# Kernel tuning notes

Hardware: AMD Instinct MI355X
Metric: run time of the kernel (lower is better)

The kernel has to match this reference:

```python
import jax, jax.numpy as jnp
import numpy as np

B, S = 256, 1024
Q_IN, K_IN, V_DIM = 256, 256, 256
KEY_DIM, N_HEADS = 64, 8


def setup_inputs() -> dict:
    key = jax.random.key(0)
    ks = jax.random.split(key, 7)
    queries = jax.random.normal(ks[0], (B, Q_IN), dtype=jnp.float32)
    keys = jax.random.normal(ks[1], (B, S, K_IN), dtype=jnp.float32)
    values = jax.random.normal(ks[2], (B, S, V_DIM), dtype=jnp.float32)
    # per-head Linear params (torch Linear: y = x @ W.T + b), stacked over heads
    sq = 1.0 / np.sqrt(Q_IN)
    sk = 1.0 / np.sqrt(K_IN)
    Wq = jax.random.uniform(ks[3], (N_HEADS, KEY_DIM, Q_IN), minval=-sq, maxval=sq, dtype=jnp.float32)
    bq = jax.random.uniform(ks[4], (N_HEADS, KEY_DIM), minval=-sq, maxval=sq, dtype=jnp.float32)
    Wk = jax.random.uniform(ks[5], (N_HEADS, KEY_DIM, K_IN), minval=-sk, maxval=sk, dtype=jnp.float32)
    bk = jax.random.uniform(ks[6], (N_HEADS, KEY_DIM), minval=-sk, maxval=sk, dtype=jnp.float32)
    return {"queries": queries, "keys": keys, "values": values,
            "Wq": Wq, "bq": bq, "Wk": Wk, "bk": bk}


def reference(queries, keys, values, Wq, bq, Wk, bk):
    # q: (B, H, D)  -- single query per batch element, per head
    q = jnp.einsum('bi,hdi->bhd', queries, Wq) + bq[None, :, :]
    # k: (B, H, S, D)
    k = jnp.einsum('bsi,hdi->bhsd', keys, Wk) + bk[None, :, None, :]
    scale = 1.0 / jnp.sqrt(jnp.float32(KEY_DIM))
    # scores: (B, H, S)
    scores = jnp.einsum('bhd,bhsd->bhs', q, k) * scale
    attn = jax.nn.softmax(scores, axis=-1)
    # out: (B, H, V); original returns (B, H, 1, V) after unsqueeze+cat
    out = jnp.einsum('bhs,bsv->bhv', attn, values)
    return out[:, :, None, :]
```

## Files before the change

### kernel.cpp

```cpp
#include <hip/hip_runtime.h>

#define NHEADS 8
#define DHEAD 64
#define CIN 256
#define SLEN 1024
#define VDIM 256
#define PT_STRIDE 1048

typedef __attribute__((ext_vector_type(8))) short bf16x8;
typedef __attribute__((ext_vector_type(4))) float f32x4;

__device__ __forceinline__ unsigned short f2bf(float x) {
    unsigned int u = __builtin_bit_cast(unsigned int, x);
    u += 0x7fffu + ((u >> 16) & 1u);
    return (unsigned short)(u >> 16);
}

extern "C" __global__ void __launch_bounds__(1024)
attn_fused_kernel(const float* __restrict__ queries,
                  const float* __restrict__ keys,
                  const float* __restrict__ values,
                  const float* __restrict__ Wq,
                  const float* __restrict__ bq,
                  const float* __restrict__ Wk,
                  const float* __restrict__ bk,
                  float* __restrict__ out)
{
    __shared__ __align__(16) float          q_lds[CIN];
    __shared__ float                        qh[NHEADS * DHEAD];
    __shared__ __align__(16) unsigned short rb[CIN * 16];
    __shared__ __align__(16) float          sc[SLEN * NHEADS];
    __shared__ __align__(16) unsigned short pT[16 * PT_STRIDE];
    __shared__ float                        red[16 * NHEADS];
    __shared__ float                        gmax[NHEADS];
    __shared__ float                        gsum[NHEADS];
    __shared__ float                        c_lds[NHEADS];

    const int b    = blockIdx.x;
    const int t    = threadIdx.x;
    const int lane = t & 63;
    const int wave = t >> 6;
    const int col  = lane & 15;
    const int kgrp = lane >> 4;

    if (t < CIN / 4) {
        ((float4*)q_lds)[t] = ((const float4*)(queries + (size_t)b * CIN))[t];
    }
    __syncthreads();

    if (t < NHEADS * DHEAD) {
        const float4* wq = (const float4*)(Wq + (size_t)t * CIN);
        const float4* q4 = (const float4*)q_lds;
        float acc = bq[t];
        #pragma unroll 8
        for (int i = 0; i < CIN / 4; ++i) {
            float4 w = wq[i], q = q4[i];
            acc += w.x * q.x + w.y * q.y + w.z * q.z + w.w * q.w;
        }
        qh[t] = acc;
    }
    __syncthreads();

    for (int idx = t; idx < NHEADS * CIN; idx += 1024) {
        int h = idx >> 8;
        int i = idx & 255;
        const float* wk = Wk + ((size_t)h * DHEAD) * CIN + i;
        float acc = 0.f;
        #pragma unroll 8
        for (int d = 0; d < DHEAD; ++d) acc += qh[h * DHEAD + d] * wk[(size_t)d * CIN];
        rb[i * 16 + h]     = f2bf(acc);
        rb[i * 16 + 8 + h] = 0;
    }
    if (t < NHEADS) {
        float acc = 0.f;
        for (int d = 0; d < DHEAD; ++d) acc += qh[t * DHEAD + d] * bk[t * DHEAD + d];
        c_lds[t] = acc;
    }
    __syncthreads();

    bf16x8 bfr[8];
    #pragma unroll
    for (int kk = 0; kk < 8; ++kk) {
        unsigned short* bp = (unsigned short*)&bfr[kk];
        #pragma unroll
        for (int j = 0; j < 8; ++j)
            bp[j] = rb[(kk * 32 + kgrp * 8 + j) * 16 + col];
    }
    const float* kbase = keys + (size_t)b * SLEN * CIN;
    for (int tile = wave; tile < SLEN / 16; tile += 16) {
        int s0 = tile * 16;
        f32x4 acc = {0.f, 0.f, 0.f, 0.f};
        const float* arow = kbase + (size_t)(s0 + col) * CIN + kgrp * 8;
        #pragma unroll
        for (int kk = 0; kk < 8; ++kk) {
            float4 a0 = *(const float4*)(arow + kk * 32);
            float4 a1 = *(const float4*)(arow + kk * 32 + 4);
            bf16x8 af;
            unsigned short* ap = (unsigned short*)&af;
            ap[0] = f2bf(a0.x); ap[1] = f2bf(a0.y); ap[2] = f2bf(a0.z); ap[3] = f2bf(a0.w);
            ap[4] = f2bf(a1.x); ap[5] = f2bf(a1.y); ap[6] = f2bf(a1.z); ap[7] = f2bf(a1.w);
            acc = __builtin_amdgcn_mfma_f32_16x16x32_bf16(af, bfr[kk], acc, 0, 0, 0);
        }
        if (col < NHEADS) {
            float c = c_lds[col];
            #pragma unroll
            for (int m = 0; m < 4; ++m)
                sc[(s0 + kgrp * 4 + m) * NHEADS + col] = (acc[m] + c) * 0.125f;
        }
    }
    __syncthreads();

    float v[8];
    {
        float4 x0 = *(const float4*)&sc[t * NHEADS + 0];
        float4 x1 = *(const float4*)&sc[t * NHEADS + 4];
        v[0] = x0.x; v[1] = x0.y; v[2] = x0.z; v[3] = x0.w;
        v[4] = x1.x; v[5] = x1.y; v[6] = x1.z; v[7] = x1.w;
    }
    float m8[8];
    #pragma unroll
    for (int h = 0; h < NHEADS; ++h) {
        float x = v[h];
        #pragma unroll
        for (int mask = 1; mask < 64; mask <<= 1)
            x = fmaxf(x, __shfl_xor(x, mask, 64));
        m8[h] = x;
    }
    if (lane == 0) {
        #pragma unroll
        for (int h = 0; h < NHEADS; ++h) red[wave * NHEADS + h] = m8[h];
    }
    __syncthreads();
    if (wave == 0) {
        int w = lane >> 3, h = lane & 7;
        float x = fmaxf(red[w * NHEADS + h], red[(w + 8) * NHEADS + h]);
        x = fmaxf(x, __shfl_xor(x, 8, 64));
        x = fmaxf(x, __shfl_xor(x, 16, 64));
        x = fmaxf(x, __shfl_xor(x, 32, 64));
        if (lane < NHEADS) gmax[lane] = x;
    }
    __syncthreads();
    float p[8];
    #pragma unroll
    for (int h = 0; h < NHEADS; ++h) {
        p[h] = __expf(v[h] - gmax[h]);
        pT[h * PT_STRIDE + t] = f2bf(p[h]);
    }
    #pragma unroll
    for (int h = 0; h < NHEADS; ++h) {
        float x = p[h];
        #pragma unroll
        for (int mask = 1; mask < 64; mask <<= 1)
            x += __shfl_xor(x, mask, 64);
        m8[h] = x;
    }
    if (lane == 0) {
        #pragma unroll
        for (int h = 0; h < NHEADS; ++h) red[wave * NHEADS + h] = m8[h];
    }
    __syncthreads();
    if (wave == 0) {
        int w = lane >> 3, h = lane & 7;
        float x = red[w * NHEADS + h] + red[(w + 8) * NHEADS + h];
        x += __shfl_xor(x, 8, 64);
        x += __shfl_xor(x, 16, 64);
        x += __shfl_xor(x, 32, 64);
        if (lane < NHEADS) gsum[lane] = x;
    }
    __syncthreads();

    {
        const int n0 = wave * 16;
        const float* vbase = values + (size_t)b * SLEN * VDIM + n0 + col;
        const unsigned short* arow = pT + col * PT_STRIDE + kgrp * 8;
        f32x4 acc = {0.f, 0.f, 0.f, 0.f};
        for (int kk = 0; kk < SLEN / 32; ++kk) {
            bf16x8 af = *(const bf16x8*)(arow + kk * 32);
            int sb = kk * 32 + kgrp * 8;
            bf16x8 bf;
            unsigned short* bp = (unsigned short*)&bf;
            #pragma unroll
            for (int j = 0; j < 8; ++j)
                bp[j] = f2bf(vbase[(size_t)(sb + j) * VDIM]);
            acc = __builtin_amdgcn_mfma_f32_16x16x32_bf16(af, bf, acc, 0, 0, 0);
        }
        int rbase = kgrp * 4;
        if (rbase < NHEADS) {
            #pragma unroll
            for (int m = 0; m < 4; ++m) {
                int h = rbase + m;
                out[(size_t)b * NHEADS * VDIM + h * VDIM + n0 + col] = acc[m] / gsum[h];
            }
        }
    }
}

extern "C" void kernel_launch(void* const* d_in, const int* in_sizes, int n_in,
                              void* d_out, int out_size, void* d_ws, size_t ws_size,
                              hipStream_t stream) {
    const float* queries = (const float*)d_in[0];
    const float* keys    = (const float*)d_in[1];
    const float* values  = (const float*)d_in[2];
    const float* Wq      = (const float*)d_in[3];
    const float* bq      = (const float*)d_in[4];
    const float* Wk      = (const float*)d_in[5];
    const float* bk      = (const float*)d_in[6];
    float* out           = (float*)d_out;
    (void)in_sizes; (void)n_in; (void)out_size; (void)d_ws; (void)ws_size;

    attn_fused_kernel<<<dim3(256), dim3(1024), 0, stream>>>(
        queries, keys, values, Wq, bq, Wk, bk, out);
}
```

Baseline: 124.7 us.

## Restructure into per-wave flash-style softmax with split-S value accumulation

Each wave now owns a contiguous 64-key chunk. It computes its scores in registers, applies a local max/exp softmax, and runs P·V for all 256 value columns on its own chunk. The partial results are then merged across waves using rescale factors from the per-wave max and sum, followed by an LDS staged reduction. This removes the LDS score buffer, the block-wide reductions, and the barriers between the score phase and the value phase, so each wave streams keys and values without waiting on the others. The costs are a large accumulator register footprint (16 f32x4), a final cross-wave LDS reduction loop, and a swizzled layout for the rb2 weight buffer.

```diff
diff --git a/kernel.cpp b/kernel.cpp
--- a/kernel.cpp
+++ b/kernel.cpp
@@ -5,7 +5,6 @@
 #define CIN 256
 #define SLEN 1024
 #define VDIM 256
-#define PT_STRIDE 1048
 
 typedef __attribute__((ext_vector_type(8))) short bf16x8;
 typedef __attribute__((ext_vector_type(4))) float f32x4;
@@ -15,9 +14,12 @@
     u += 0x7fffu + ((u >> 16) & 1u);
     return (unsigned short)(u >> 16);
 }
-
-extern "C" __global__ void __launch_bounds__(1024)
-attn_fused_kernel(const float* __restrict__ queries,
+__device__ __forceinline__ unsigned int pack2bf(float lo, float hi) {
+    return (unsigned int)f2bf(lo) | ((unsigned int)f2bf(hi) << 16);
+}
+
+extern "C" __global__ void __launch_bounds__(1024, 4)
+attn_flash_kernel(const float* __restrict__ queries,
                   const float* __restrict__ keys,
                   const float* __restrict__ values,
                   const float* __restrict__ Wq,
@@ -28,13 +30,13 @@
 {
     __shared__ __align__(16) float          q_lds[CIN];
     __shared__ float                        qh[NHEADS * DHEAD];
-    __shared__ __align__(16) unsigned short rb[CIN * 16];
-    __shared__ __align__(16) float          sc[SLEN * NHEADS];
-    __shared__ __align__(16) unsigned short pT[16 * PT_STRIDE];
-    __shared__ float                        red[16 * NHEADS];
-    __shared__ float                        gmax[NHEADS];
-    __shared__ float                        gsum[NHEADS];
-    __shared__ float                        c_lds[NHEADS];
+    __shared__ __align__(16) unsigned short rb2[16 * 256];
+    __shared__ float                        c16[16];
+    __shared__ float                        wm[16][8];
+    __shared__ float                        wl[16][8];
+    __shared__ float                        wf[16][8];
+    __shared__ float                        ML[16];
+    __shared__ __align__(16) float          stage[16][8][64];
 
     const int b    = blockIdx.x;
     const int t    = threadIdx.x;
@@ -68,29 +70,31 @@
         float acc = 0.f;
         #pragma unroll 8
         for (int d = 0; d < DHEAD; ++d) acc += qh[h * DHEAD + d] * wk[(size_t)d * CIN];
-        rb[i * 16 + h]     = f2bf(acc);
-        rb[i * 16 + 8 + h] = 0;
-    }
-    if (t < NHEADS) {
+        rb2[h * 256 + (i ^ ((h & 7) << 3))] = f2bf(acc);
+        rb2[2048 + idx] = 0;
+    }
+    if (t < 16) {
         float acc = 0.f;
-        for (int d = 0; d < DHEAD; ++d) acc += qh[t * DHEAD + d] * bk[t * DHEAD + d];
-        c_lds[t] = acc;
-    }
-    __syncthreads();
+        if (t < 8) {
+            for (int d = 0; d < DHEAD; ++d) acc += qh[t * DHEAD + d] * bk[t * DHEAD + d];
+        }
+        c16[t] = acc;
+    }
+    __syncthreads();
+
+    const int wbase = wave * 64;
 
     bf16x8 bfr[8];
     #pragma unroll
-    for (int kk = 0; kk < 8; ++kk) {
-        unsigned short* bp = (unsigned short*)&bfr[kk];
-        #pragma unroll
-        for (int j = 0; j < 8; ++j)
-            bp[j] = rb[(kk * 32 + kgrp * 8 + j) * 16 + col];
-    }
+    for (int kk = 0; kk < 8; ++kk)
+        bfr[kk] = *(const bf16x8*)&rb2[col * 256 + ((kk * 32 + kgrp * 8) ^ ((col & 7) << 3))];
+
+    f32x4 sacc[4];
     const float* kbase = keys + (size_t)b * SLEN * CIN;
-    for (int tile = wave; tile < SLEN / 16; tile += 16) {
-        int s0 = tile * 16;
+    #pragma unroll
+    for (int tile = 0; tile < 4; ++tile) {
+        const float* arow = kbase + (size_t)(wbase + tile * 16 + col) * CIN + kgrp * 8;
         f32x4 acc = {0.f, 0.f, 0.f, 0.f};
-        const float* arow = kbase + (size_t)(s0 + col) * CIN + kgrp * 8;
         #pragma unroll
         for (int kk = 0; kk < 8; ++kk) {
             float4 a0 = *(const float4*)(arow + kk * 32);
@@ -101,97 +105,120 @@
             ap[4] = f2bf(a1.x); ap[5] = f2bf(a1.y); ap[6] = f2bf(a1.z); ap[7] = f2bf(a1.w);
             acc = __builtin_amdgcn_mfma_f32_16x16x32_bf16(af, bfr[kk], acc, 0, 0, 0);
         }
-        if (col < NHEADS) {
-            float c = c_lds[col];
-            #pragma unroll
-            for (int m = 0; m < 4; ++m)
-                sc[(s0 + kgrp * 4 + m) * NHEADS + col] = (acc[m] + c) * 0.125f;
-        }
-    }
-    __syncthreads();
-
-    float v[8];
+        sacc[tile] = acc;
+    }
+
     {
-        float4 x0 = *(const float4*)&sc[t * NHEADS + 0];
-        float4 x1 = *(const float4*)&sc[t * NHEADS + 4];
-        v[0] = x0.x; v[1] = x0.y; v[2] = x0.z; v[3] = x0.w;
-        v[4] = x1.x; v[5] = x1.y; v[6] = x1.z; v[7] = x1.w;
-    }
-    float m8[8];
-    #pragma unroll
-    for (int h = 0; h < NHEADS; ++h) {
-        float x = v[h];
-        #pragma unroll
-        for (int mask = 1; mask < 64; mask <<= 1)
-            x = fmaxf(x, __shfl_xor(x, mask, 64));
-        m8[h] = x;
-    }
-    if (lane == 0) {
-        #pragma unroll
-        for (int h = 0; h < NHEADS; ++h) red[wave * NHEADS + h] = m8[h];
-    }
-    __syncthreads();
-    if (wave == 0) {
-        int w = lane >> 3, h = lane & 7;
-        float x = fmaxf(red[w * NHEADS + h], red[(w + 8) * NHEADS + h]);
-        x = fmaxf(x, __shfl_xor(x, 8, 64));
-        x = fmaxf(x, __shfl_xor(x, 16, 64));
-        x = fmaxf(x, __shfl_xor(x, 32, 64));
-        if (lane < NHEADS) gmax[lane] = x;
-    }
-    __syncthreads();
-    float p[8];
-    #pragma unroll
-    for (int h = 0; h < NHEADS; ++h) {
-        p[h] = __expf(v[h] - gmax[h]);
-        pT[h * PT_STRIDE + t] = f2bf(p[h]);
-    }
-    #pragma unroll
-    for (int h = 0; h < NHEADS; ++h) {
-        float x = p[h];
-        #pragma unroll
-        for (int mask = 1; mask < 64; mask <<= 1)
-            x += __shfl_xor(x, mask, 64);
-        m8[h] = x;
-    }
-    if (lane == 0) {
-        #pragma unroll
-        for (int h = 0; h < NHEADS; ++h) red[wave * NHEADS + h] = m8[h];
-    }
-    __syncthreads();
-    if (wave == 0) {
-        int w = lane >> 3, h = lane & 7;
-        float x = red[w * NHEADS + h] + red[(w + 8) * NHEADS + h];
-        x += __shfl_xor(x, 8, 64);
-        x += __shfl_xor(x, 16, 64);
-        x += __shfl_xor(x, 32, 64);
-        if (lane < NHEADS) gsum[lane] = x;
-    }
-    __syncthreads();
-
-    {
-        const int n0 = wave * 16;
-        const float* vbase = values + (size_t)b * SLEN * VDIM + n0 + col;
-        const unsigned short* arow = pT + col * PT_STRIDE + kgrp * 8;
-        f32x4 acc = {0.f, 0.f, 0.f, 0.f};
-        for (int kk = 0; kk < SLEN / 32; ++kk) {
-            bf16x8 af = *(const bf16x8*)(arow + kk * 32);
-            int sb = kk * 32 + kgrp * 8;
-            bf16x8 bf;
-            unsigned short* bp = (unsigned short*)&bf;
-            #pragma unroll
-            for (int j = 0; j < 8; ++j)
-                bp[j] = f2bf(vbase[(size_t)(sb + j) * VDIM]);
-            acc = __builtin_amdgcn_mfma_f32_16x16x32_bf16(af, bf, acc, 0, 0, 0);
-        }
-        int rbase = kgrp * 4;
-        if (rbase < NHEADS) {
+        float c = c16[col];
+        float mw = -1e30f;
+        #pragma unroll
+        for (int tile = 0; tile < 4; ++tile) {
             #pragma unroll
             for (int m = 0; m < 4; ++m) {
-                int h = rbase + m;
-                out[(size_t)b * NHEADS * VDIM + h * VDIM + n0 + col] = acc[m] / gsum[h];
+                float s = (sacc[tile][m] + c) * 0.125f;
+                sacc[tile][m] = s;
+                mw = fmaxf(mw, s);
             }
         }
+        mw = fmaxf(mw, __shfl_xor(mw, 16, 64));
+        mw = fmaxf(mw, __shfl_xor(mw, 32, 64));
+        float lw = 0.f;
+        #pragma unroll
+        for (int tile = 0; tile < 4; ++tile) {
+            #pragma unroll
+            for (int m = 0; m < 4; ++m) {
+                float p = __expf(sacc[tile][m] - mw);
+                sacc[tile][m] = p;
+                lw += p;
+            }
+        }
+        lw += __shfl_xor(lw, 16, 64);
+        lw += __shfl_xor(lw, 32, 64);
+        if (kgrp == 0 && col < 8) {
+            wm[wave][col] = mw;
+            wl[wave][col] = lw;
+        }
+    }
+
+    unsigned int pw[8];
+    #pragma unroll
+    for (int tile = 0; tile < 4; ++tile) {
+        pw[tile * 2 + 0] = pack2bf(sacc[tile][0], sacc[tile][1]);
+        pw[tile * 2 + 1] = pack2bf(sacc[tile][2], sacc[tile][3]);
+    }
+
+    f32x4 acc[16];
+    #pragma unroll
+    for (int n = 0; n < 16; ++n) acc[n] = (f32x4){0.f, 0.f, 0.f, 0.f};
+
+    const float* vbase = values + (size_t)b * SLEN * VDIM + col;
+    #pragma unroll
+    for (int kk = 0; kk < 2; ++kk) {
+        bf16x8 af;
+        unsigned int* aw = (unsigned int*)&af;
+        #pragma unroll
+        for (int jj = 0; jj < 4; ++jj) {
+            int srcLane = col + 16 * ((kgrp & 1) * 2 + (jj >> 1));
+            unsigned int lo = (unsigned int)__shfl((int)pw[4 * kk + (jj & 1)], srcLane, 64);
+            unsigned int hi = (unsigned int)__shfl((int)pw[4 * kk + 2 + (jj & 1)], srcLane, 64);
+            aw[jj] = (kgrp & 2) ? hi : lo;
+        }
+        const float* rp = vbase + (size_t)(wbase + kk * 32 + kgrp * 8) * VDIM;
+        #pragma unroll
+        for (int n = 0; n < 16; ++n) {
+            float v0 = rp[0 * VDIM + n * 16];
+            float v1 = rp[1 * VDIM + n * 16];
+            float v2 = rp[2 * VDIM + n * 16];
+            float v3 = rp[3 * VDIM + n * 16];
+            float v4 = rp[4 * VDIM + n * 16];
+            float v5 = rp[5 * VDIM + n * 16];
+            float v6 = rp[6 * VDIM + n * 16];
+            float v7 = rp[7 * VDIM + n * 16];
+            bf16x8 bv;
+            unsigned short* bp = (unsigned short*)&bv;
+            bp[0] = f2bf(v0); bp[1] = f2bf(v1); bp[2] = f2bf(v2); bp[3] = f2bf(v3);
+            bp[4] = f2bf(v4); bp[5] = f2bf(v5); bp[6] = f2bf(v6); bp[7] = f2bf(v7);
+            acc[n] = __builtin_amdgcn_mfma_f32_16x16x32_bf16(af, bv, acc[n], 0, 0, 0);
+        }
+    }
+
+    __syncthreads();
+
+    if (t < 8) {
+        float M = -1e30f;
+        for (int w = 0; w < 16; ++w) M = fmaxf(M, wm[w][t]);
+        float L = 0.f;
+        for (int w = 0; w < 16; ++w) L += wl[w][t] * __expf(wm[w][t] - M);
+        ML[t] = M;
+        ML[8 + t] = L;
+    }
+    __syncthreads();
+    if (t < 128) {
+        int w = t >> 3, h = t & 7;
+        wf[w][h] = __expf(wm[w][h] - ML[h]) / ML[8 + h];
+    }
+    __syncthreads();
+
+    #pragma unroll
+    for (int cch = 0; cch < 4; ++cch) {
+        if (kgrp < 2) {
+            #pragma unroll
+            for (int tl = 0; tl < 4; ++tl) {
+                int n = cch * 4 + tl;
+                #pragma unroll
+                for (int m = 0; m < 4; ++m)
+                    stage[wave][kgrp * 4 + m][tl * 16 + col] = acc[n][m] * wf[wave][kgrp * 4 + m];
+            }
+        }
+        __syncthreads();
+        if (t < 512) {
+            int h = t >> 6, vl = t & 63;
+            float o = 0.f;
+            #pragma unroll
+            for (int w = 0; w < 16; ++w) o += stage[w][h][vl];
+            out[(size_t)b * NHEADS * VDIM + h * VDIM + cch * 64 + vl] = o;
+        }
+        __syncthreads();
     }
 }
 
@@ -208,6 +235,6 @@
     float* out           = (float*)d_out;
     (void)in_sizes; (void)n_in; (void)out_size; (void)d_ws; (void)ws_size;
 
-    attn_fused_kernel<<<dim3(256), dim3(1024), 0, stream>>>(
+    attn_flash_kernel<<<dim3(256), dim3(1024), 0, stream>>>(
         queries, keys, values, Wq, bq, Wk, bk, out);
 }
```

Measured after the change: 171.3 us. +37.4%, slower.
